# Kernel tuning notes

Measured on AMD Instinct MI355X. Metric: run time of the kernel, lower is better.

The kernel has to match this reference:

```python
import jax, jax.numpy as jnp
import numpy as np

NUM_CHANNEL_TYPES = 32  # global channel vocabulary (matches fill_max of channel_idx)


def setup_inputs() -> dict:
    key = jax.random.key(0)
    k1, k2, k3, k4, k5, k6 = jax.random.split(key, 6)
    B, C, H, W, E, P = 32, 8, 224, 224, 768, 16
    return {
        "x": jax.random.normal(k1, (B, C, H, W), dtype=jnp.float32),
        "channel_idx": jax.random.randint(k2, (B, C), 0, NUM_CHANNEL_TYPES, dtype=jnp.int64),
        "proj_w": jax.random.normal(k3, (E, P, P), dtype=jnp.float32) * 0.02,
        "proj_b": jax.random.normal(k4, (E,), dtype=jnp.float32) * 0.02,
        "ctx_w": jax.random.normal(k5, (E, E), dtype=jnp.float32) * 0.02,
        "ctx_b": jax.random.normal(k6, (E,), dtype=jnp.float32) * 0.02,
    }


def reference(x, channel_idx, proj_w, proj_b, ctx_w, ctx_b):
    B, C, H, W = x.shape
    E, P, _ = proj_w.shape
    Hp, Wp = H // P, W // P

    # Conv3d(1, E, kernel=(1,P,P), stride=(1,P,P)) == per-channel 2D patchify matmul
    xp = x.reshape(B, C, Hp, P, Wp, P)
    emb = jnp.einsum('bchpwq,epq->bechw', xp, proj_w) + proj_b[None, :, None, None, None]
    # emb: (B, E, C, Hp, Wp)

    # per-(sample, channel) average patch embedding -> (B, C, E)
    av_patch = emb.mean(axis=(3, 4)).transpose(0, 2, 1)
    flat = av_patch.reshape(B * C, E)
    seg = channel_idx.reshape(-1)

    # segment-mean over the batch by channel index (fused scatter-mean)
    sums = jax.ops.segment_sum(flat, seg, num_segments=NUM_CHANNEL_TYPES)
    cnt = jax.ops.segment_sum(jnp.ones((B * C,), flat.dtype), seg, num_segments=NUM_CHANNEL_TYPES)
    means = sums / jnp.maximum(cnt, 1.0)[:, None]
    chan_embed = means[seg].reshape(B, C, E)  # torch computes this under no_grad

    # context projection and broadcast-add back onto patch embeddings
    ctx = chan_embed @ ctx_w.T + ctx_b            # (B, C, E)
    out = emb + ctx.transpose(0, 2, 1)[:, :, :, None, None]

    # flatten(2).transpose(1, 2): (B, C*Hp*Wp, E)
    return out.reshape(B, E, C * Hp * Wp).transpose(0, 2, 1)
```

## Files before the change

kernel.cpp:

```cpp
#include <hip/hip_runtime.h>
#include <hip/hip_bf16.h>

typedef __attribute__((ext_vector_type(8))) short s16x8;
typedef __attribute__((ext_vector_type(4))) float f32x4;
typedef __attribute__((ext_vector_type(8))) unsigned short u16x8;
typedef __attribute__((ext_vector_type(4))) unsigned short u16x4;

static __device__ __forceinline__ unsigned short f2bf(float f) {
  unsigned int u = __float_as_uint(f);
  unsigned int r = u + 0x7fffu + ((u >> 16) & 1u);
  return (unsigned short)(r >> 16);
}
static __device__ __forceinline__ float bf2f(unsigned short s) {
  return __uint_as_float(((unsigned int)s) << 16);
}

static __device__ __forceinline__ void gload16(const void* g, void* l) {
  __builtin_amdgcn_global_load_lds(
      (const __attribute__((address_space(1))) unsigned int*)g,
      (__attribute__((address_space(3))) unsigned int*)l, 16, 0, 0);
}

__global__ __launch_bounds__(256) void k_mega(const float* __restrict__ x,
                                              unsigned short* __restrict__ xbf,
                                              float* __restrict__ avg3,
                                              const float* __restrict__ pw,
                                              unsigned short* __restrict__ pwbf,
                                              const float* __restrict__ cw,
                                              float* __restrict__ cwT) {
  __shared__ __align__(16) char smem[14 * 272 * 2];
  int b = blockIdx.x, t = threadIdx.x;
  if (b < 3584) {
    unsigned short* strip = (unsigned short*)smem;
    int bc = b / 14, hp = b - bc * 14;
    const float* img = x + ((size_t)bc * 224 + hp * 16) * 224;
    for (int idx = t; idx < 896; idx += 256) {
      int row = idx / 56, c4 = idx - row * 56;
      float4 v = reinterpret_cast<const float4*>(img + (size_t)row * 224)[c4];
      int wp = c4 >> 2, q0 = (c4 & 3) << 2;
      u16x4 pk = { f2bf(v.x), f2bf(v.y), f2bf(v.z), f2bf(v.w) };
      *(u16x4*)&strip[wp * 272 + row * 16 + q0] = pk;
    }
    __syncthreads();
    float acc = 0.f;
#pragma unroll
    for (int wp = 0; wp < 14; ++wp) acc += bf2f(strip[wp * 272 + t]);
    avg3[((size_t)bc * 14 + hp) * 256 + t] = acc;
    unsigned short* orow = xbf + ((size_t)bc * 196 + hp * 14) * 256;
    for (int i = t; i < 448; i += 256) {
      int patch = i >> 5, rem = i & 31;
      u16x8 v = *(const u16x8*)&strip[patch * 272 + (rem >> 1) * 16 + (rem & 1) * 8];
      *(u16x8*)(orow + i * 8) = v;
    }
  } else if (b < 3776) {
    int i = (b - 3584) * 256 + t;
    float4 v = reinterpret_cast<const float4*>(pw)[i];
    u16x4 pk = { f2bf(v.x), f2bf(v.y), f2bf(v.z), f2bf(v.w) };
    reinterpret_cast<u16x4*>(pwbf)[i] = pk;
  } else {
    float (*tile)[33] = (float(*)[33])smem;
    int bid2 = b - 3776;
    int bx = bid2 % 24, by = bid2 / 24;
    int tx = t & 31, ty = t >> 5;
#pragma unroll
    for (int k = 0; k < 4; ++k)
      tile[ty + 8 * k][tx] = cw[(size_t)(by * 32 + ty + 8 * k) * 768 + bx * 32 + tx];
    __syncthreads();
#pragma unroll
    for (int k = 0; k < 4; ++k)
      cwT[(size_t)(bx * 32 + ty + 8 * k) * 768 + by * 32 + tx] = tile[tx][ty + 8 * k];
  }
}

__global__ __launch_bounds__(256) void k_segmean(const float* __restrict__ avg3,
                                                 const int* __restrict__ seg,
                                                 float* __restrict__ sp) {
  __shared__ float red[4][64];
  __shared__ int rcnt[4];
  __shared__ int ssg[256];
  int s = blockIdx.x & 31, kc = blockIdx.x >> 5;
  int t = threadIdx.x;
  int kl = t & 63, slice = t >> 6;
  int k = kc * 64 + kl;
  ssg[t] = seg[t];
  __syncthreads();
  float sum = 0.f; int cnt = 0;
  for (int bc = slice * 64; bc < slice * 64 + 64; ++bc) {
    if (ssg[bc] == s) {
      ++cnt;
      const float* row = avg3 + (size_t)bc * 14 * 256 + k;
#pragma unroll
      for (int hp = 0; hp < 14; ++hp) sum += row[hp * 256];
    }
  }
  red[slice][kl] = sum;
  if (kl == 0) rcnt[slice] = cnt;
  __syncthreads();
  if (t < 64) {
    float tot = red[0][t] + red[1][t] + red[2][t] + red[3][t];
    int c = rcnt[0] + rcnt[1] + rcnt[2] + rcnt[3];
    sp[s * 256 + kc * 64 + t] = tot / (196.0f * (float)(c > 0 ? c : 1));
  }
}

__global__ __launch_bounds__(256) void k_means2(const float* __restrict__ sp,
                                                const float* __restrict__ pw,
                                                const float* __restrict__ pb,
                                                float* __restrict__ means) {
  __shared__ float ssp[256];
  __shared__ float red[8][32];
  int s = blockIdx.x & 31, e0 = (blockIdx.x >> 5) << 5;
  int t = threadIdx.x;
  int e = t & 31, ksl = t >> 5;
  ssp[t] = sp[s * 256 + t];
  __syncthreads();
  const float4* w = reinterpret_cast<const float4*>(pw + (size_t)(e0 + e) * 256 + ksl * 32);
  float a = 0.f;
#pragma unroll
  for (int j = 0; j < 8; ++j) {
    float4 v = w[j];
    int kb = ksl * 32 + j * 4;
    a += v.x * ssp[kb] + v.y * ssp[kb + 1] + v.z * ssp[kb + 2] + v.w * ssp[kb + 3];
  }
  red[ksl][e] = a;
  __syncthreads();
  if (t < 32) {
    float tot = 0.f;
#pragma unroll
    for (int j = 0; j < 8; ++j) tot += red[j][t];
    means[s * 768 + e0 + t] = tot + pb[e0 + t];
  }
}

__global__ __launch_bounds__(256) void k_ctx2(const float* __restrict__ means,
                                              const float* __restrict__ cwT,
                                              const float* __restrict__ cb,
                                              const float* __restrict__ pb,
                                              float* __restrict__ addv) {
  __shared__ float mn[768];
  __shared__ float red[8][32];
  int s = blockIdx.x & 31, e0 = (blockIdx.x >> 5) << 5;
  int t = threadIdx.x;
  int e = t & 31, fsl = t >> 5;
  mn[t] = means[s * 768 + t];
  mn[t + 256] = means[s * 768 + 256 + t];
  mn[t + 512] = means[s * 768 + 512 + t];
  __syncthreads();
  const float* col = cwT + (size_t)fsl * 96 * 768 + e0 + e;
  float a = 0.f;
#pragma unroll 8
  for (int j = 0; j < 96; ++j) a += mn[fsl * 96 + j] * col[(size_t)j * 768];
  red[fsl][e] = a;
  __syncthreads();
  if (t < 32) {
    float tot = 0.f;
#pragma unroll
    for (int j = 0; j < 8; ++j) tot += red[j][t];
    addv[s * 768 + e0 + t] = tot + cb[e0 + t] + pb[e0 + t];
  }
}

__global__ __launch_bounds__(256) void k_gemm(
    const unsigned short* __restrict__ xbf, const unsigned short* __restrict__ wbf,
    const float* __restrict__ addv, const int* __restrict__ seg,
    float* __restrict__ out) {
  __shared__ __align__(16) unsigned short Al[3][128 * 32];
  __shared__ __align__(16) unsigned short Bl[3][128 * 32];

  int bid = blockIdx.x;
  int xcd = bid & 7, local = bid >> 3;
  int mb = xcd * 49 + local / 6;
  int nb = local - (local / 6) * 6;
  int m0 = mb << 7, n0 = nb << 7;

  int t = threadIdx.x;
  int wave = t >> 6, lane = t & 63;
  int wm = (wave >> 1) << 6, wn = (wave & 1) << 6;
  int lr = lane & 15, hi = lane >> 4;

  int srcq = ((lane & 3) ^ ((lane >> 3) & 3)) << 4;
  const char* abase0 = (const char*)xbf + (size_t)(m0 + wave * 32 + (lane >> 2)) * 512 + srcq;
  const char* bbase0 = (const char*)wbf + (size_t)(n0 + wave * 32 + (lane >> 2)) * 512 + srcq;
  int ldso = wave * 2048 + (lane & 31) * 16 + ((lane >> 5) << 10);
  (void)ldso;

#define STAGE(kt_, buf_)                                                        \
  do {                                                                          \
    const char* an = abase0 + (kt_) * 64;                                       \
    const char* bn = bbase0 + (kt_) * 64;                                       \
    gload16(an,         (char*)Al[buf_] + wave * 2048 + (lane << 4));           \
    gload16(an + 8192,  (char*)Al[buf_] + wave * 2048 + 1024 + (lane << 4));    \
    gload16(bn,         (char*)Bl[buf_] + wave * 2048 + (lane << 4));           \
    gload16(bn + 8192,  (char*)Bl[buf_] + wave * 2048 + 1024 + (lane << 4));    \
  } while (0)

  f32x4 acc[4][4] = {};

  STAGE(0, 0);
  STAGE(1, 1);

  int rq = (hi ^ ((lr >> 1) & 3)) << 4;

#pragma unroll
  for (int kt = 0; kt < 8; ++kt) {
    if (kt < 7) {
      asm volatile("s_waitcnt vmcnt(4)" ::: "memory");
    } else {
      asm volatile("s_waitcnt vmcnt(0)" ::: "memory");
    }
    __builtin_amdgcn_s_barrier();
    if (kt + 2 < 8) {
      int nb3 = (kt + 2) % 3;
      STAGE(kt + 2, nb3);
    }
    int cur = kt % 3;
    s16x8 af[4], bv[4];
#pragma unroll
    for (int i = 0; i < 4; ++i)
      af[i] = *(const s16x8*)((const char*)Al[cur] + (wm + i * 16 + lr) * 64 + rq);
#pragma unroll
    for (int j = 0; j < 4; ++j)
      bv[j] = *(const s16x8*)((const char*)Bl[cur] + (wn + j * 16 + lr) * 64 + rq);
#pragma unroll
    for (int i = 0; i < 4; ++i)
#pragma unroll
      for (int j = 0; j < 4; ++j)
        acc[i][j] = __builtin_amdgcn_mfma_f32_16x16x32_bf16(bv[j], af[i], acc[i][j], 0, 0, 0);
  }
#undef STAGE

#pragma unroll
  for (int i = 0; i < 4; ++i) {
    int M = m0 + wm + i * 16 + lr;
    int sgi = seg[M / 196];
    const float* av = addv + (size_t)sgi * 768 + n0 + wn + hi * 4;
    float* orow = out + (size_t)M * 768 + n0 + wn + hi * 4;
#pragma unroll
    for (int j = 0; j < 4; ++j) {
      f32x4 a4 = *(const f32x4*)(av + j * 16);
      f32x4 v = acc[i][j];
      v.x += a4.x; v.y += a4.y; v.z += a4.z; v.w += a4.w;
      *(f32x4*)(orow + j * 16) = v;
    }
  }
}

__global__ void k_cvt_fb(const float* __restrict__ in, unsigned short* __restrict__ o) {
  int i = blockIdx.x * 256 + threadIdx.x;
  float4 v = reinterpret_cast<const float4*>(in)[i];
  u16x4 pk = { f2bf(v.x), f2bf(v.y), f2bf(v.z), f2bf(v.w) };
  reinterpret_cast<u16x4*>(o)[i] = pk;
}

__global__ void k_transpose_fb(const float* __restrict__ in, float* __restrict__ out) {
  __shared__ float tile[32][33];
  int bx = blockIdx.x % 24, by = blockIdx.x / 24;
  int tx = threadIdx.x & 31, ty = threadIdx.x >> 5;
#pragma unroll
  for (int k = 0; k < 4; ++k)
    tile[ty + 8 * k][tx] = in[(size_t)(by * 32 + ty + 8 * k) * 768 + bx * 32 + tx];
  __syncthreads();
#pragma unroll
  for (int k = 0; k < 4; ++k)
    out[(size_t)(bx * 32 + ty + 8 * k) * 768 + by * 32 + tx] = tile[tx][ty + 8 * k];
}

__global__ void k_avgpatch_fb(const float* __restrict__ x, float* __restrict__ avg) {
  int bc = blockIdx.x;
  int k = threadIdx.x;
  int p = k >> 4, q = k & 15;
  const float* base = x + (size_t)bc * 224 * 224;
  float s = 0.f;
  for (int hp = 0; hp < 14; ++hp) {
    const float* row = base + (hp * 16 + p) * 224 + q;
#pragma unroll
    for (int wp = 0; wp < 14; ++wp) s += row[wp * 16];
  }
  avg[bc * 256 + k] = s * (1.0f / 196.0f);
}

__global__ __launch_bounds__(768) void k_chain_fb(const float* __restrict__ avg,
                                                  const int* __restrict__ seg,
                                                  const float* __restrict__ pw,
                                                  const float* __restrict__ pb,
                                                  const float* __restrict__ cwT,
                                                  const float* __restrict__ cb,
                                                  float* __restrict__ addv) {
  __shared__ float sp[256];
  __shared__ float mn[768];
  __shared__ int ssg[256];
  int s = blockIdx.x, t = threadIdx.x;
  if (t < 256) ssg[t] = seg[t];
  __syncthreads();
  if (t < 256) {
    float sum = 0.f; int c = 0;
    for (int bc = 0; bc < 256; ++bc)
      if (ssg[bc] == s) { sum += avg[bc * 256 + t]; ++c; }
    sp[t] = sum / (float)(c > 0 ? c : 1);
  }
  __syncthreads();
  {
    const float4* w = reinterpret_cast<const float4*>(pw + (size_t)t * 256);
    float a = 0.f;
#pragma unroll 8
    for (int k = 0; k < 64; ++k) {
      float4 v = w[k];
      a += v.x * sp[k * 4] + v.y * sp[k * 4 + 1] + v.z * sp[k * 4 + 2] + v.w * sp[k * 4 + 3];
    }
    mn[t] = a + pb[t];
  }
  __syncthreads();
  float a2 = 0.f;
#pragma unroll 8
  for (int f = 0; f < 768; ++f) a2 += mn[f] * cwT[(size_t)f * 768 + t];
  addv[s * 768 + t] = a2 + cb[t] + pb[t];
}

__global__ __launch_bounds__(256) void k_gemm_fb(
    const float* __restrict__ x, const unsigned short* __restrict__ wbf,
    const float* __restrict__ addv, const int* __restrict__ seg,
    float* __restrict__ out) {
  __shared__ unsigned short Al[128][40];
  __shared__ unsigned short Bl[128][40];
  int bid = blockIdx.x;
  int xcd = bid & 7, local = bid >> 3;
  int mb = xcd * 49 + local / 6;
  int nb = local - (local / 6) * 6;
  int m0 = mb << 7, n0 = nb << 7;
  int t = threadIdx.x;
  int wave = t >> 6, lane = t & 63;
  int wm = (wave >> 1) << 6, wn = (wave & 1) << 6;
  int lr = lane & 15, lk = (lane >> 4) << 3;
  int mstage = m0 + (t >> 1);
  int halfA = t & 1;
  int bc = mstage / 196;
  int pij = mstage - bc * 196;
  int hp = pij / 14;
  int wp = pij - hp * 14;
  const float* xbase = x + ((size_t)bc * 224 + hp * 16 + halfA) * 224 + wp * 16;
  const unsigned short* bsrc = wbf + (size_t)(n0 + (t >> 1)) * 256 + halfA * 16;
  unsigned short* adst = &Al[t >> 1][halfA * 16];
  unsigned short* bdst = &Bl[t >> 1][halfA * 16];
  f32x4 acc[4][4] = {};
  for (int ks = 0; ks < 8; ++ks) {
    __syncthreads();
    *(u16x8*)bdst       = *(const u16x8*)(bsrc + ks * 32);
    *(u16x8*)(bdst + 8) = *(const u16x8*)(bsrc + ks * 32 + 8);
    {
      const float4* src = reinterpret_cast<const float4*>(xbase + ks * 448);
      float4 v0 = src[0], v1 = src[1], v2 = src[2], v3 = src[3];
      u16x8 p0 = { f2bf(v0.x), f2bf(v0.y), f2bf(v0.z), f2bf(v0.w),
                   f2bf(v1.x), f2bf(v1.y), f2bf(v1.z), f2bf(v1.w) };
      u16x8 p1 = { f2bf(v2.x), f2bf(v2.y), f2bf(v2.z), f2bf(v2.w),
                   f2bf(v3.x), f2bf(v3.y), f2bf(v3.z), f2bf(v3.w) };
      *(u16x8*)adst = p0;
      *(u16x8*)(adst + 8) = p1;
    }
    __syncthreads();
    s16x8 af[4], bfv[4];
#pragma unroll
    for (int i = 0; i < 4; ++i) af[i] = *(const s16x8*)&Al[wm + i * 16 + lr][lk];
#pragma unroll
    for (int j = 0; j < 4; ++j) bfv[j] = *(const s16x8*)&Bl[wn + j * 16 + lr][lk];
#pragma unroll
    for (int i = 0; i < 4; ++i)
#pragma unroll
      for (int j = 0; j < 4; ++j)
        acc[i][j] = __builtin_amdgcn_mfma_f32_16x16x32_bf16(bfv[j], af[i], acc[i][j], 0, 0, 0);
  }
#pragma unroll
  for (int i = 0; i < 4; ++i) {
    int M = m0 + wm + i * 16 + lr;
    int sgi = seg[M / 196];
    int hi = lane >> 4;
    const float* av = addv + (size_t)sgi * 768 + n0 + wn + hi * 4;
    float* orow = out + (size_t)M * 768 + n0 + wn + hi * 4;
#pragma unroll
    for (int j = 0; j < 4; ++j) {
      f32x4 a4 = *(const f32x4*)(av + j * 16);
      f32x4 v = acc[i][j];
      v.x += a4.x; v.y += a4.y; v.z += a4.z; v.w += a4.w;
      *(f32x4*)(orow + j * 16) = v;
    }
  }
}


extern "C" void kernel_launch(void* const* d_in, const int* in_sizes, int n_in,
                              void* d_out, int out_size, void* d_ws, size_t ws_size,
                              hipStream_t stream) {
  (void)in_sizes; (void)n_in; (void)out_size;
  const float* x  = (const float*)d_in[0];
  const int*   sg = (const int*)d_in[1];
  const float* pw = (const float*)d_in[2];
  const float* pb = (const float*)d_in[3];
  const float* cw = (const float*)d_in[4];
  const float* cb = (const float*)d_in[5];
  float* out = (float*)d_out;

  char* ws = (char*)d_ws;
  unsigned short* pwbf = (unsigned short*)ws;
  float* cwT   = (float*)(ws + 393216);
  float* addv  = (float*)(ws + 2752512);
  float* sp    = (float*)(ws + 2850816);
  float* means = (float*)(ws + 2883584);
  float* avg3  = (float*)(ws + 2981888);
  unsigned short* xbf = (unsigned short*)(ws + 6651904);
  const size_t NEED = 6651904u + 25690112u;

  if (ws_size >= NEED) {
    k_mega<<<4352, 256, 0, stream>>>(x, xbf, avg3, pw, pwbf, cw, cwT);
    k_segmean<<<128, 256, 0, stream>>>(avg3, sg, sp);
    k_means2<<<768, 256, 0, stream>>>(sp, pw, pb, means);
    k_ctx2<<<768, 256, 0, stream>>>(means, cwT, cb, pb, addv);
    k_gemm<<<2352, 256, 0, stream>>>(xbf, pwbf, addv, sg, out);
  } else {
    float* avgp = (float*)(ws + 2981888);
    k_cvt_fb<<<192, 256, 0, stream>>>(pw, pwbf);
    k_transpose_fb<<<576, 256, 0, stream>>>(cw, cwT);
    k_avgpatch_fb<<<256, 256, 0, stream>>>(x, avgp);
    k_chain_fb<<<32, 768, 0, stream>>>(avgp, sg, pw, pb, cwT, cb, addv);
    k_gemm_fb<<<2352, 256, 0, stream>>>(x, pwbf, addv, sg, out);
  }
}
```

Baseline: 89.75 us.

## Fuse fp32-to-bf16 patch conversion into GEMM A-tile loading, drop xbf buffer

The front kernel no longer writes a bf16 patch-major copy of x. It only computes the per-patch pixel sums, using fp32 staging in shared memory. The GEMM now loads fp32 x directly into registers, converts it to bf16 and writes swizzled A tiles into a double-buffered LDS area, while B still uses async global-to-LDS loads. This removes the 25MB bf16 intermediate write and read-back. In exchange, the GEMM reads twice the A bytes from x, and register-staged A loading may expose more latency than async LDS loads.

Result: slower. 93.26 us (+3.9%).

```diff
diff --git a/kernel.cpp b/kernel.cpp
--- a/kernel.cpp
+++ b/kernel.cpp
@@ -11,9 +11,6 @@
   unsigned int r = u + 0x7fffu + ((u >> 16) & 1u);
   return (unsigned short)(r >> 16);
 }
-static __device__ __forceinline__ float bf2f(unsigned short s) {
-  return __uint_as_float(((unsigned int)s) << 16);
-}
 
 static __device__ __forceinline__ void gload16(const void* g, void* l) {
   __builtin_amdgcn_global_load_lds(
@@ -21,37 +18,28 @@
       (__attribute__((address_space(3))) unsigned int*)l, 16, 0, 0);
 }
 
-__global__ __launch_bounds__(256) void k_mega(const float* __restrict__ x,
-                                              unsigned short* __restrict__ xbf,
-                                              float* __restrict__ avg3,
-                                              const float* __restrict__ pw,
-                                              unsigned short* __restrict__ pwbf,
-                                              const float* __restrict__ cw,
-                                              float* __restrict__ cwT) {
-  __shared__ __align__(16) char smem[14 * 272 * 2];
+__global__ __launch_bounds__(256) void k_front(const float* __restrict__ x,
+                                               float* __restrict__ avg3,
+                                               const float* __restrict__ pw,
+                                               unsigned short* __restrict__ pwbf,
+                                               const float* __restrict__ cw,
+                                               float* __restrict__ cwT) {
+  __shared__ __align__(16) float smem[16 * 228];
   int b = blockIdx.x, t = threadIdx.x;
   if (b < 3584) {
-    unsigned short* strip = (unsigned short*)smem;
     int bc = b / 14, hp = b - bc * 14;
     const float* img = x + ((size_t)bc * 224 + hp * 16) * 224;
     for (int idx = t; idx < 896; idx += 256) {
       int row = idx / 56, c4 = idx - row * 56;
       float4 v = reinterpret_cast<const float4*>(img + (size_t)row * 224)[c4];
-      int wp = c4 >> 2, q0 = (c4 & 3) << 2;
-      u16x4 pk = { f2bf(v.x), f2bf(v.y), f2bf(v.z), f2bf(v.w) };
-      *(u16x4*)&strip[wp * 272 + row * 16 + q0] = pk;
+      *(float4*)&smem[row * 228 + c4 * 4] = v;
     }
     __syncthreads();
+    int p = t >> 4, q = t & 15;
     float acc = 0.f;
 #pragma unroll
-    for (int wp = 0; wp < 14; ++wp) acc += bf2f(strip[wp * 272 + t]);
+    for (int wp = 0; wp < 14; ++wp) acc += smem[p * 228 + wp * 16 + q];
     avg3[((size_t)bc * 14 + hp) * 256 + t] = acc;
-    unsigned short* orow = xbf + ((size_t)bc * 196 + hp * 14) * 256;
-    for (int i = t; i < 448; i += 256) {
-      int patch = i >> 5, rem = i & 31;
-      u16x8 v = *(const u16x8*)&strip[patch * 272 + (rem >> 1) * 16 + (rem & 1) * 8];
-      *(u16x8*)(orow + i * 8) = v;
-    }
   } else if (b < 3776) {
     int i = (b - 3584) * 256 + t;
     float4 v = reinterpret_cast<const float4*>(pw)[i];
@@ -161,11 +149,11 @@
 }
 
 __global__ __launch_bounds__(256) void k_gemm(
-    const unsigned short* __restrict__ xbf, const unsigned short* __restrict__ wbf,
+    const float* __restrict__ x, const unsigned short* __restrict__ wbf,
     const float* __restrict__ addv, const int* __restrict__ seg,
     float* __restrict__ out) {
-  __shared__ __align__(16) unsigned short Al[3][128 * 32];
-  __shared__ __align__(16) unsigned short Bl[3][128 * 32];
+  __shared__ __align__(16) unsigned short LA[2][128 * 32];
+  __shared__ __align__(16) unsigned short LB[3][128 * 32];
 
   int bid = blockIdx.x;
   int xcd = bid & 7, local = bid >> 3;
@@ -178,56 +166,87 @@
   int wm = (wave >> 1) << 6, wn = (wave & 1) << 6;
   int lr = lane & 15, hi = lane >> 4;
 
+  int P = t >> 1, h = t & 1;
+  int gm = m0 + P;
+  int bcP = gm / 196;
+  int rem = gm - bcP * 196;
+  int hpP = rem / 14;
+  int wpP = rem - hpP * 14;
+  const float* xb = x + ((size_t)bcP * 224 + hpP * 16 + h) * 224 + wpP * 16;
+  int fA = (P + (P >> 2)) & 3;
+  int c0 = ((2 * h) ^ fA) << 4;
+  int c1 = ((2 * h + 1) ^ fA) << 4;
+  int laRow = P * 64;
+
   int srcq = ((lane & 3) ^ ((lane >> 3) & 3)) << 4;
-  const char* abase0 = (const char*)xbf + (size_t)(m0 + wave * 32 + (lane >> 2)) * 512 + srcq;
   const char* bbase0 = (const char*)wbf + (size_t)(n0 + wave * 32 + (lane >> 2)) * 512 + srcq;
-  int ldso = wave * 2048 + (lane & 31) * 16 + ((lane >> 5) << 10);
-  (void)ldso;
-
-#define STAGE(kt_, buf_)                                                        \
-  do {                                                                          \
-    const char* an = abase0 + (kt_) * 64;                                       \
-    const char* bn = bbase0 + (kt_) * 64;                                       \
-    gload16(an,         (char*)Al[buf_] + wave * 2048 + (lane << 4));           \
-    gload16(an + 8192,  (char*)Al[buf_] + wave * 2048 + 1024 + (lane << 4));    \
-    gload16(bn,         (char*)Bl[buf_] + wave * 2048 + (lane << 4));           \
-    gload16(bn + 8192,  (char*)Bl[buf_] + wave * 2048 + 1024 + (lane << 4));    \
+
+  int rqa = ((lr + (lr >> 2)) & 3) << 4;
+  int rqb = ((lr >> 1) & 3) << 4;
+
+  f32x4 acc[4][4] = {};
+  float4 ra[2][4];
+
+#define ISSUE_A(kt_)                                                           \
+  do {                                                                         \
+    const float4* s_ = reinterpret_cast<const float4*>(xb + (kt_) * 448);      \
+    ra[(kt_) & 1][0] = s_[0]; ra[(kt_) & 1][1] = s_[1];                        \
+    ra[(kt_) & 1][2] = s_[2]; ra[(kt_) & 1][3] = s_[3];                        \
   } while (0)
 
-  f32x4 acc[4][4] = {};
-
-  STAGE(0, 0);
-  STAGE(1, 1);
-
-  int rq = (hi ^ ((lr >> 1) & 3)) << 4;
+#define ISSUE_B(kt_)                                                           \
+  do {                                                                         \
+    const char* bn_ = bbase0 + (kt_) * 64;                                     \
+    char* d_ = (char*)LB[(kt_) % 3] + wave * 2048;                             \
+    gload16(bn_, d_);                                                          \
+    gload16(bn_ + 8192, d_ + 1024);                                            \
+  } while (0)
+
+#define WRITE_A(kt_)                                                           \
+  do {                                                                         \
+    float4 v0 = ra[(kt_) & 1][0], v1 = ra[(kt_) & 1][1];                       \
+    float4 v2 = ra[(kt_) & 1][2], v3 = ra[(kt_) & 1][3];                       \
+    u16x8 lo = { f2bf(v0.x), f2bf(v0.y), f2bf(v0.z), f2bf(v0.w),               \
+                 f2bf(v1.x), f2bf(v1.y), f2bf(v1.z), f2bf(v1.w) };             \
+    u16x8 hi8 = { f2bf(v2.x), f2bf(v2.y), f2bf(v2.z), f2bf(v2.w),              \
+                  f2bf(v3.x), f2bf(v3.y), f2bf(v3.z), f2bf(v3.w) };            \
+    char* base_ = (char*)LA[(kt_) & 1] + laRow;                                \
+    *(u16x8*)(base_ + c0) = lo;                                                \
+    *(u16x8*)(base_ + c1) = hi8;                                               \
+  } while (0)
+
+  ISSUE_A(0);
+  ISSUE_B(0);
 
 #pragma unroll
   for (int kt = 0; kt < 8; ++kt) {
+    WRITE_A(kt);
     if (kt < 7) {
-      asm volatile("s_waitcnt vmcnt(4)" ::: "memory");
+      ISSUE_A(kt + 1);
+      ISSUE_B(kt + 1);
+      asm volatile("s_waitcnt vmcnt(6) lgkmcnt(0)" ::: "memory");
     } else {
-      asm volatile("s_waitcnt vmcnt(0)" ::: "memory");
+      asm volatile("s_waitcnt vmcnt(0) lgkmcnt(0)" ::: "memory");
     }
     __builtin_amdgcn_s_barrier();
-    if (kt + 2 < 8) {
-      int nb3 = (kt + 2) % 3;
-      STAGE(kt + 2, nb3);
-    }
-    int cur = kt % 3;
+    const char* A_ = (const char*)LA[kt & 1];
+    const char* B_ = (const char*)LB[kt % 3];
     s16x8 af[4], bv[4];
 #pragma unroll
     for (int i = 0; i < 4; ++i)
-      af[i] = *(const s16x8*)((const char*)Al[cur] + (wm + i * 16 + lr) * 64 + rq);
+      af[i] = *(const s16x8*)(A_ + (wm + i * 16 + lr) * 64 + ((hi << 4) ^ rqa));
 #pragma unroll
     for (int j = 0; j < 4; ++j)
-      bv[j] = *(const s16x8*)((const char*)Bl[cur] + (wn + j * 16 + lr) * 64 + rq);
+      bv[j] = *(const s16x8*)(B_ + (wn + j * 16 + lr) * 64 + ((hi << 4) ^ rqb));
 #pragma unroll
     for (int i = 0; i < 4; ++i)
 #pragma unroll
       for (int j = 0; j < 4; ++j)
         acc[i][j] = __builtin_amdgcn_mfma_f32_16x16x32_bf16(bv[j], af[i], acc[i][j], 0, 0, 0);
   }
-#undef STAGE
+#undef ISSUE_A
+#undef ISSUE_B
+#undef WRITE_A
 
 #pragma unroll
   for (int i = 0; i < 4; ++i) {
@@ -405,15 +424,14 @@
   float* sp    = (float*)(ws + 2850816);
   float* means = (float*)(ws + 2883584);
   float* avg3  = (float*)(ws + 2981888);
-  unsigned short* xbf = (unsigned short*)(ws + 6651904);
-  const size_t NEED = 6651904u + 25690112u;
+  const size_t NEED = 2981888u + 3670016u;
 
   if (ws_size >= NEED) {
-    k_mega<<<4352, 256, 0, stream>>>(x, xbf, avg3, pw, pwbf, cw, cwT);
+    k_front<<<4352, 256, 0, stream>>>(x, avg3, pw, pwbf, cw, cwT);
     k_segmean<<<128, 256, 0, stream>>>(avg3, sg, sp);
     k_means2<<<768, 256, 0, stream>>>(sp, pw, pb, means);
     k_ctx2<<<768, 256, 0, stream>>>(means, cwT, cb, pb, addv);
-    k_gemm<<<2352, 256, 0, stream>>>(xbf, pwbf, addv, sg, out);
+    k_gemm<<<2352, 256, 0, stream>>>(x, pwbf, addv, sg, out);
   } else {
     float* avgp = (float*)(ws + 2981888);
     k_cvt_fb<<<192, 256, 0, stream>>>(pw, pwbf);
```
